# Performance work log

Hardware: AMD Instinct MI355X
Metric: run time of the kernel (lower is better)

## Reference

```python
import jax, jax.numpy as jnp
import numpy as np

N_IN, N_REC, T, BATCH = 128, 512, 1000, 64
ALPHA = 0.2
SIGMA = float(np.sqrt(2.0 / ALPHA) * 0.05)  # sqrt(2/alpha)*sigma_rec
EI_RATIO = 0.8
W_REC_GAIN = 1.0


def setup_inputs() -> dict:
    key = jax.random.key(0)
    k_x, k_n = jax.random.split(key)
    rng = np.random.RandomState(0)
    # w_in init: randn/sqrt(n_in)
    w_in = (rng.randn(N_IN, N_REC) / np.sqrt(N_IN)).astype(np.float32)
    # w_rec init 'randgauss' with Dale's law: abs, inhibitory rows scaled
    n_ex = int(N_REC * EI_RATIO)
    w_rec0 = W_REC_GAIN * rng.randn(N_REC, N_REC) / np.sqrt(N_REC)
    w_rec0 = np.abs(w_rec0)
    w_rec0[n_ex:, :] *= EI_RATIO / (1.0 - EI_RATIO)
    w_rec = w_rec0.astype(np.float32)
    ei_vec = np.concatenate([np.ones(n_ex), -np.ones(N_REC - n_ex)]).astype(np.float32)
    ei_mask = np.diag(ei_vec)
    autapse_mask = np.ones((N_REC, N_REC), dtype=np.float32)
    np.fill_diagonal(autapse_mask, 0.0)
    x = jax.random.normal(k_x, (BATCH, T, N_IN), dtype=jnp.float32)
    # pre-scaled noise: randn * sigma, one draw per timestep (matches torch.randn_like(h)*sigma)
    noise = jax.random.normal(k_n, (BATCH, T, N_REC), dtype=jnp.float32) * SIGMA
    return {
        "x": x,
        "w_in": jnp.asarray(w_in),
        "w_rec": jnp.asarray(w_rec),
        "b_rec": jnp.zeros((N_REC,), dtype=jnp.float32),
        "ei_mask": jnp.asarray(ei_mask),
        "autapse_mask": jnp.asarray(autapse_mask),
        "noise": noise,
    }


def reference(x, w_in, w_rec, b_rec, ei_mask, autapse_mask, noise):
    # Effective recurrent weight, computed ONCE (torch code recomputes each step)
    w_eff = ei_mask @ (w_rec * autapse_mask)          # (n_rec, n_rec)
    inp_all = jnp.einsum("bti,ir->btr", x, w_in)       # precompute input projection
    xs = (jnp.swapaxes(inp_all, 0, 1), jnp.swapaxes(noise, 0, 1))  # (T,b,r)
    h0 = jnp.zeros((x.shape[0], w_rec.shape[0]), dtype=x.dtype)

    def step(h, xt):
        inp_t, noise_t = xt
        pre = inp_t + h @ w_eff + b_rec + noise_t
        h_new = (1.0 - ALPHA) * h + ALPHA * jax.nn.relu(pre)
        return h_new, h_new

    _, h_all = jax.lax.scan(step, h0, xs)              # (T, batch, n_rec)
    return jnp.swapaxes(h_all, 0, 1)                   # (batch, T, n_rec)
```

## Files before the change

### kernel.cpp

```cpp
#include <hip/hip_runtime.h>

#define T_STEPS 1000
#define NIN     128
#define NREC    512
#define NBATCH  64
#define ALPHA   0.2f

#define NSLICE  4
#define SCOLS   128
#define NGRP    8
#define KPER    64

#define WS_W_OFF     0
#define WS_COMM_OFF  (1u << 20)
#define COMM_U64     (NBATCH * NREC)
#define WS_NEEDED    (WS_COMM_OFF + 2 * COMM_U64 * 8)

__global__ void weff_kernel(const float* __restrict__ w_rec,
                            const float* __restrict__ ei_mask,
                            const float* __restrict__ autapse,
                            float* __restrict__ w_eff) {
    int idx = blockIdx.x * blockDim.x + threadIdx.x;
    if (idx < NREC * NREC) {
        int row = idx >> 9;
        float ei = ei_mask[row * NREC + row];
        w_eff[idx] = ei * w_rec[idx] * autapse[idx];
    }
}

__global__ __launch_bounds__(1024) void gemm_in_kernel(
        const float* __restrict__ x,
        const float* __restrict__ w_in,
        const float* __restrict__ b_rec,
        float* __restrict__ io) {
    __shared__ float xs[32][NIN];

    const int tid = threadIdx.x;
    const int m0  = blockIdx.x * 32;

    {
        const float4* src = reinterpret_cast<const float4*>(x + (size_t)m0 * NIN);
        reinterpret_cast<float4*>(&xs[0][0])[tid] = src[tid];
    }
    __syncthreads();

    const int j0 = tid & 255;
    const int j1 = j0 + 256;
    const int rg = tid >> 8;

    float acc[8][2];
#pragma unroll
    for (int i = 0; i < 8; ++i) { acc[i][0] = 0.f; acc[i][1] = 0.f; }

#pragma unroll 4
    for (int k = 0; k < NIN; ++k) {
        float wv0 = w_in[k * NREC + j0];
        float wv1 = w_in[k * NREC + j1];
#pragma unroll
        for (int i = 0; i < 8; ++i) {
            float xv = xs[rg * 8 + i][k];
            acc[i][0] = fmaf(xv, wv0, acc[i][0]);
            acc[i][1] = fmaf(xv, wv1, acc[i][1]);
        }
    }

    const float br0 = b_rec[j0];
    const float br1 = b_rec[j1];
#pragma unroll
    for (int i = 0; i < 8; ++i) {
        size_t ro = (size_t)(m0 + rg * 8 + i) * NREC;
        io[ro + j0] = acc[i][0] + br0;
        io[ro + j1] = acc[i][1] + br1;
    }
}

__global__ __launch_bounds__(1024, 4) void rnn_coop(
        const float* __restrict__ W,
        const float* __restrict__ noise,
        float* __restrict__ io,
        unsigned long long* __restrict__ comm) {
    __shared__ __align__(16) float h_lds[NREC];
    __shared__ float part[NGRP * SCOLS];

    const int tid = threadIdx.x;
    const int b   = blockIdx.x >> 2;
    const int s   = blockIdx.x & 3;
    const int jl  = tid & (SCOLS - 1);
    const int g   = tid >> 7;
    const int ln  = tid & 63;
    const int jg  = s * SCOLS + jl;
    const bool remote = (g >> 1) != s;
    const int cslot = g * KPER + ln;

    float Wr[KPER];
    {
        const float* wp = W + (size_t)(g * KPER) * NREC + jg;
#pragma unroll
        for (int u = 0; u < KPER; ++u)
            Wr[u] = wp[(size_t)u * NREC];
    }
#pragma unroll
    for (int u = 0; u < KPER; ++u)
        asm volatile("" : "+v"(Wr[u]));

    if (tid < NREC) h_lds[tid] = 0.f;
    __syncthreads();

    float hj = 0.f;
    const size_t iobase = (size_t)b * T_STEPS * NREC + jg;
    const unsigned long long* cbase = comm + (size_t)b * NREC + cslot;
    unsigned long long* cwbase = comm + (size_t)b * NREC + jg;

    for (int t = 0; t < T_STEPS; ++t) {
        const size_t off = iobase + (size_t)t * NREC;
        float inp = 0.f, nz = 0.f;
        if (tid < SCOLS) { inp = io[off]; nz = noise[off]; }

        if (t > 0 && remote) {
            const unsigned long long* cp = cbase + (size_t)(t & 1) * COMM_U64;
            unsigned long long v = __hip_atomic_load(
                cp, __ATOMIC_RELAXED, __HIP_MEMORY_SCOPE_AGENT);
            while ((int)(unsigned)(v >> 32) < t)
                v = __hip_atomic_load(cp, __ATOMIC_RELAXED,
                                      __HIP_MEMORY_SCOPE_AGENT);
            asm volatile("" ::: "memory");
            h_lds[cslot] = __uint_as_float((unsigned)(v & 0xffffffffu));
        }

        float a0 = 0.f, a1 = 0.f, a2 = 0.f, a3 = 0.f;
        const float4* h4 = reinterpret_cast<const float4*>(&h_lds[g * KPER]);
#pragma unroll
        for (int u = 0; u < KPER / 4; ++u) {
            float4 hv = h4[u];
            a0 = fmaf(hv.x, Wr[4 * u + 0], a0);
            a1 = fmaf(hv.y, Wr[4 * u + 1], a1);
            a2 = fmaf(hv.z, Wr[4 * u + 2], a2);
            a3 = fmaf(hv.w, Wr[4 * u + 3], a3);
        }
        part[g * SCOLS + jl] = (a0 + a1) + (a2 + a3);
        __syncthreads();

        if (tid < SCOLS) {
            float pre = inp + nz;
#pragma unroll
            for (int q = 0; q < NGRP; ++q)
                pre += part[q * SCOLS + jl];
            float hnew = (1.f - ALPHA) * hj + ALPHA * fmaxf(pre, 0.f);
            hj = hnew;
            h_lds[jg] = hnew;
            unsigned long long pv =
                ((unsigned long long)(unsigned)(t + 1) << 32) |
                (unsigned long long)__float_as_uint(hnew);
            __hip_atomic_store(cwbase + (size_t)((t + 1) & 1) * COMM_U64, pv,
                               __ATOMIC_RELAXED, __HIP_MEMORY_SCOPE_AGENT);
            io[off] = hnew;
        }
        __syncthreads();
    }
}

__global__ __launch_bounds__(1024) void rnn_kernel(
        const float* __restrict__ W,
        const float* __restrict__ noise,
        float* __restrict__ io) {
    __shared__ float h[NREC];
    __shared__ float part2[NREC];

    const int tid  = threadIdx.x;
    const int j    = tid & (NREC - 1);
    const int half = tid >> 9;
    const int b    = blockIdx.x;

    if (tid < NREC) h[tid] = 0.f;
    float hj = 0.f;
    __syncthreads();

    const int kb = half * 256;
    const float* wp = W + (size_t)kb * NREC + j;
    const size_t base = (size_t)b * T_STEPS * NREC + j;

    for (int t = 0; t < T_STEPS; ++t) {
        const size_t off = base + (size_t)t * NREC;
        float acc = (half == 0) ? (io[off] + noise[off]) : 0.f;
#pragma unroll
        for (int ku = 0; ku < 256; ku += 16) {
            float w[16];
#pragma unroll
            for (int u = 0; u < 16; ++u) w[u] = wp[(size_t)(ku + u) * NREC];
#pragma unroll
            for (int u = 0; u < 16; ++u) acc = fmaf(h[kb + ku + u], w[u], acc);
        }
        if (half == 1) part2[j] = acc;
        __syncthreads();
        if (half == 0) {
            float pre  = acc + part2[j];
            float hnew = (1.f - ALPHA) * hj + ALPHA * fmaxf(pre, 0.f);
            io[off] = hnew;
            h[j] = hnew;
            hj = hnew;
        }
        __syncthreads();
    }
}

extern "C" void kernel_launch(void* const* d_in, const int* in_sizes, int n_in,
                              void* d_out, int out_size, void* d_ws, size_t ws_size,
                              hipStream_t stream) {
    const float* x       = (const float*)d_in[0];
    const float* w_in    = (const float*)d_in[1];
    const float* w_rec   = (const float*)d_in[2];
    const float* b_rec   = (const float*)d_in[3];
    const float* ei_mask = (const float*)d_in[4];
    const float* autapse = (const float*)d_in[5];
    const float* noise   = (const float*)d_in[6];
    float* out = (float*)d_out;

    char* ws = (char*)d_ws;
    float* W = (float*)(ws + WS_W_OFF);
    unsigned long long* comm = (unsigned long long*)(ws + WS_COMM_OFF);

    weff_kernel<<<dim3((NREC * NREC + 255) / 256), dim3(256), 0, stream>>>(
        w_rec, ei_mask, autapse, W);

    gemm_in_kernel<<<dim3(64000 / 32), dim3(1024), 0, stream>>>(
        x, w_in, b_rec, out);

    if (ws_size >= (size_t)WS_NEEDED) {
        hipMemsetAsync(comm, 0, 2 * COMM_U64 * 8, stream);
        void* args[] = {(void*)&W, (void*)&noise, (void*)&out, (void*)&comm};
        hipLaunchCooperativeKernel(reinterpret_cast<void*>(rnn_coop),
                                   dim3(NBATCH * NSLICE), dim3(1024),
                                   args, 0, stream);
    } else {
        rnn_kernel<<<dim3(NBATCH), dim3(1024), 0, stream>>>(W, noise, out);
    }
}
```

Before: 1.684 ms.

## Pipeline RNN step with double-buffered partials and a single barrier

Each step of the cooperative recurrent kernel is restructured so the reduction and state update for step t-1 happen at the start of step t, reading double-buffered partial sums. This removes one block-wide barrier per timestep. Every wave now fetches its whole h slice from the global comm buffer into a private LDS stage, so no cross-wave sharing of h is needed. Input and noise values for the next step are prefetched, and the barrier becomes a raw s_barrier after an LDS waitcnt. The cost is that even locally produced h values now make a round trip through L2 polling, and there is an extra epilogue for the final step.

After: 1.833 ms. 1.09x slower.

```diff
diff --git a/kernel.cpp b/kernel.cpp
--- a/kernel.cpp
+++ b/kernel.cpp
@@ -15,6 +15,12 @@
 #define WS_COMM_OFF  (1u << 20)
 #define COMM_U64     (NBATCH * NREC)
 #define WS_NEEDED    (WS_COMM_OFF + 2 * COMM_U64 * 8)
+
+#define LDS_BARRIER() do {                                        \
+    asm volatile("s_waitcnt lgkmcnt(0)" ::: "memory");            \
+    __builtin_amdgcn_s_barrier();                                 \
+    asm volatile("" ::: "memory");                                \
+} while (0)
 
 __global__ void weff_kernel(const float* __restrict__ w_rec,
                             const float* __restrict__ ei_mask,
@@ -79,8 +85,8 @@
         const float* __restrict__ noise,
         float* __restrict__ io,
         unsigned long long* __restrict__ comm) {
-    __shared__ __align__(16) float h_lds[NREC];
-    __shared__ float part[NGRP * SCOLS];
+    __shared__ __align__(16) float h_stage[NREC];
+    __shared__ float part[2][NGRP * SCOLS];
 
     const int tid = threadIdx.x;
     const int b   = blockIdx.x >> 2;
@@ -89,8 +95,6 @@
     const int g   = tid >> 7;
     const int ln  = tid & 63;
     const int jg  = s * SCOLS + jl;
-    const bool remote = (g >> 1) != s;
-    const int cslot = g * KPER + ln;
 
     float Wr[KPER];
     {
@@ -103,32 +107,46 @@
     for (int u = 0; u < KPER; ++u)
         asm volatile("" : "+v"(Wr[u]));
 
-    if (tid < NREC) h_lds[tid] = 0.f;
-    __syncthreads();
-
     float hj = 0.f;
     const size_t iobase = (size_t)b * T_STEPS * NREC + jg;
-    const unsigned long long* cbase = comm + (size_t)b * NREC + cslot;
+    const unsigned long long* cbase = comm + (size_t)b * NREC + g * KPER + ln;
     unsigned long long* cwbase = comm + (size_t)b * NREC + jg;
 
+    float inp = 0.f, nz = 0.f;
+    if (tid < SCOLS) { inp = io[iobase]; nz = noise[iobase]; }
+
     for (int t = 0; t < T_STEPS; ++t) {
-        const size_t off = iobase + (size_t)t * NREC;
-        float inp = 0.f, nz = 0.f;
-        if (tid < SCOLS) { inp = io[off]; nz = noise[off]; }
-
-        if (t > 0 && remote) {
-            const unsigned long long* cp = cbase + (size_t)(t & 1) * COMM_U64;
-            unsigned long long v = __hip_atomic_load(
-                cp, __ATOMIC_RELAXED, __HIP_MEMORY_SCOPE_AGENT);
-            while ((int)(unsigned)(v >> 32) < t)
-                v = __hip_atomic_load(cp, __ATOMIC_RELAXED,
-                                      __HIP_MEMORY_SCOPE_AGENT);
-            asm volatile("" ::: "memory");
-            h_lds[cslot] = __uint_as_float((unsigned)(v & 0xffffffffu));
-        }
+        const int p = t & 1;
+
+        const unsigned long long* cp = cbase + (size_t)p * COMM_U64;
+        unsigned long long v = __hip_atomic_load(
+            cp, __ATOMIC_RELAXED, __HIP_MEMORY_SCOPE_AGENT);
+
+        if (t > 0 && tid < SCOLS) {
+            float pre = inp + nz;
+#pragma unroll
+            for (int q = 0; q < NGRP; ++q)
+                pre += part[p ^ 1][q * SCOLS + jl];
+            float hnew = (1.f - ALPHA) * hj + ALPHA * fmaxf(pre, 0.f);
+            hj = hnew;
+            unsigned long long pv =
+                ((unsigned long long)(unsigned)t << 32) |
+                (unsigned long long)__float_as_uint(hnew);
+            __hip_atomic_store(cwbase + (size_t)p * COMM_U64, pv,
+                               __ATOMIC_RELAXED, __HIP_MEMORY_SCOPE_AGENT);
+            io[iobase + (size_t)(t - 1) * NREC] = hnew;
+            inp = io[iobase + (size_t)t * NREC];
+            nz  = noise[iobase + (size_t)t * NREC];
+        }
+
+        while ((int)(unsigned)(v >> 32) < t)
+            v = __hip_atomic_load(cp, __ATOMIC_RELAXED,
+                                  __HIP_MEMORY_SCOPE_AGENT);
+        asm volatile("" ::: "memory");
+        h_stage[g * KPER + ln] = __uint_as_float((unsigned)(v & 0xffffffffu));
 
         float a0 = 0.f, a1 = 0.f, a2 = 0.f, a3 = 0.f;
-        const float4* h4 = reinterpret_cast<const float4*>(&h_lds[g * KPER]);
+        const float4* h4 = reinterpret_cast<const float4*>(&h_stage[g * KPER]);
 #pragma unroll
         for (int u = 0; u < KPER / 4; ++u) {
             float4 hv = h4[u];
@@ -137,25 +155,19 @@
             a2 = fmaf(hv.z, Wr[4 * u + 2], a2);
             a3 = fmaf(hv.w, Wr[4 * u + 3], a3);
         }
-        part[g * SCOLS + jl] = (a0 + a1) + (a2 + a3);
-        __syncthreads();
-
-        if (tid < SCOLS) {
-            float pre = inp + nz;
-#pragma unroll
-            for (int q = 0; q < NGRP; ++q)
-                pre += part[q * SCOLS + jl];
-            float hnew = (1.f - ALPHA) * hj + ALPHA * fmaxf(pre, 0.f);
-            hj = hnew;
-            h_lds[jg] = hnew;
-            unsigned long long pv =
-                ((unsigned long long)(unsigned)(t + 1) << 32) |
-                (unsigned long long)__float_as_uint(hnew);
-            __hip_atomic_store(cwbase + (size_t)((t + 1) & 1) * COMM_U64, pv,
-                               __ATOMIC_RELAXED, __HIP_MEMORY_SCOPE_AGENT);
-            io[off] = hnew;
-        }
-        __syncthreads();
+        part[p][g * SCOLS + jl] = (a0 + a1) + (a2 + a3);
+
+        LDS_BARRIER();
+    }
+
+    if (tid < SCOLS) {
+        const int pe = (T_STEPS - 1) & 1;
+        float pre = inp + nz;
+#pragma unroll
+        for (int q = 0; q < NGRP; ++q)
+            pre += part[pe][q * SCOLS + jl];
+        float hnew = (1.f - ALPHA) * hj + ALPHA * fmaxf(pre, 0.f);
+        io[iobase + (size_t)(T_STEPS - 1) * NREC] = hnew;
     }
 }
 
```
